# Kernel tuning notes

Measured on AMD Instinct MI355X. Metric: run time of the kernel, lower is better.

## Reference

```python
import jax, jax.numpy as jnp
import numpy as np
from jax import lax

NPOINT = 1024
NSAMPLE = 32
RADIUS = 0.6
BN_EPS = 1e-5


def square_distance(src, dst):
    # src (B,S,3), dst (B,N,3) -> (B,S,N) squared distances
    d = -2.0 * jnp.einsum('bsc,bnc->bsn', src, dst)
    d = d + jnp.sum(src ** 2, -1)[:, :, None]
    d = d + jnp.sum(dst ** 2, -1)[:, None, :]
    return d


def farthest_point_sample(xyz, npoint):
    B, N, _ = xyz.shape
    bidx = jnp.arange(B)

    def step(carry, _):
        distance, farthest = carry
        centroid = xyz[bidx, farthest]                      # (B,3)
        dist = jnp.sum((xyz - centroid[:, None, :]) ** 2, -1)  # (B,N)
        distance = jnp.minimum(distance, dist)
        new_far = jnp.argmax(distance, -1)
        return (distance, new_far), farthest

    init = (jnp.full((B, N), 1e10, xyz.dtype), jnp.zeros((B,), jnp.int32))
    _, idxs = lax.scan(step, init, None, length=npoint)
    return idxs.T                                            # (B,npoint)


def ball_query(xyz, new_xyz, radius, nsample):
    B, N, _ = xyz.shape
    sqr = square_distance(new_xyz, xyz)                      # (B,S,N)
    idx = jnp.where(sqr <= radius ** 2, jnp.arange(N)[None, None, :], N)
    idx = jnp.sort(idx, axis=-1)[:, :, :nsample]             # (B,S,K)
    first = idx[:, :, :1]
    return jnp.where(idx == N, first, idx)


def gather2(points, idx):
    # points (B,N,C), idx (B,S) -> (B,S,C)
    return jax.vmap(lambda p, i: p[i])(points, idx)


def gather3(points, idx):
    # points (B,N,C), idx (B,S,K) -> (B,S,K,C)
    return jax.vmap(lambda p, i: p[i])(points, idx)


def sa_forward(xyz, features, params):
    fps_idx = lax.stop_gradient(farthest_point_sample(xyz, NPOINT))
    new_xyz = gather2(xyz, fps_idx)                          # (B,S,3)
    idx = lax.stop_gradient(ball_query(xyz, new_xyz, RADIUS, NSAMPLE))
    grouped_xyz = gather3(xyz, idx) - new_xyz[:, :, None, :] # (B,S,K,3)
    grouped_feat = gather3(features.transpose(0, 2, 1), idx) # (B,S,K,C)
    g = jnp.concatenate([grouped_xyz, grouped_feat], -1)     # (B,S,K,C+3)
    g = g.transpose(0, 3, 2, 1)                              # (B,Cin,K,S)
    for w, b, ga, be in params:
        g = jnp.einsum('oc,bcks->boks', w, g) + b[None, :, None, None]
        mu = jnp.mean(g, axis=(0, 2, 3), keepdims=True)
        var = jnp.var(g, axis=(0, 2, 3), keepdims=True)
        g = ga[None, :, None, None] * (g - mu) * lax.rsqrt(var + BN_EPS) \
            + be[None, :, None, None]
        g = jax.nn.relu(g)
    new_features = jnp.max(g, axis=2)                        # (B,Cout,S)
    return new_xyz, new_features


def setup_inputs() -> dict:
    key = jax.random.key(0)
    ks = jax.random.split(key, 8)
    B, N, C = 16, 4096, 128
    cin = C + 3
    mlp = [128, 128, 256]
    inp = {
        'xyz': jax.random.normal(ks[0], (B, N, 3), jnp.float32),
        'features': jax.random.normal(ks[1], (B, C, N), jnp.float32),
    }
    prev = cin
    for i, out in enumerate(mlp):
        inp[f'w{i}'] = jax.random.normal(ks[2 + i], (out, prev), jnp.float32) * 0.05
        inp[f'b{i}'] = jnp.zeros((out,), jnp.float32)
        inp[f'gamma{i}'] = jnp.ones((out,), jnp.float32)
        inp[f'beta{i}'] = jnp.zeros((out,), jnp.float32)
        prev = out
    return inp


def reference(xyz, features, w0, b0, gamma0, beta0, w1, b1, gamma1, beta1,
              w2, b2, gamma2, beta2):
    params = [(w0, b0, gamma0, beta0), (w1, b1, gamma1, beta1),
              (w2, b2, gamma2, beta2)]
    return sa_forward(xyz, features, params)
```

## Files before the change

kernel.cpp:

```cpp
#include <hip/hip_runtime.h>

#define B_ 16
#define N_ 4096
#define S_ 1024
#define K_ 32
#define PITCH2 136
#define PITCH1 168

typedef unsigned long long u64;
typedef short bf16x8 __attribute__((ext_vector_type(8)));
typedef unsigned short u16x8 __attribute__((ext_vector_type(8)));
typedef float f32x4 __attribute__((ext_vector_type(4)));
typedef float f32x2 __attribute__((ext_vector_type(2)));

__device__ __forceinline__ unsigned short f2bf(float f) {
  unsigned u = __float_as_uint(f);
  unsigned r = (u + 0x7FFFu + ((u >> 16) & 1u)) >> 16;
  return (unsigned short)r;
}
__device__ __forceinline__ float bf2f(unsigned short h) {
  return __uint_as_float(((unsigned)h) << 16);
}

#define DPP_MAX(v, ctrl)                                                        \
  {                                                                             \
    int _t = __builtin_amdgcn_update_dpp(__float_as_int(v), __float_as_int(v),  \
                                         ctrl, 0xf, 0xf, false);                \
    v = fmaxf(v, __int_as_float(_t));                                           \
  }

__global__ __launch_bounds__(512) void k_front(
    const float* __restrict__ xyz, float* __restrict__ new_xyz,
    const float* __restrict__ feat, unsigned short* __restrict__ featT,
    const float* __restrict__ w0, const float* __restrict__ w1,
    const float* __restrict__ w2, unsigned short* __restrict__ wbf0,
    unsigned short* __restrict__ wbf1, unsigned short* __restrict__ wbf2,
    float* __restrict__ stats) {
  __shared__ __align__(16) float smem[N_ * 4 + S_ + 64];
  int blk = blockIdx.x, t = threadIdx.x;

  if (blk < 16) {
#pragma clang fp contract(off)
#if __has_builtin(__builtin_amdgcn_s_setprio)
    __builtin_amdgcn_s_setprio(3);
#endif
    float4* pts = (float4*)smem;
    int* idxs = (int*)(smem + N_ * 4);
    u64* km = (u64*)(smem + N_ * 4 + S_);
    int b = blk;
    const float* base = xyz + (size_t)b * N_ * 3;
    for (int i = t; i < N_; i += 512)
      pts[i] = make_float4(base[i * 3], base[i * 3 + 1], base[i * 3 + 2], 0.0f);
    if (t == 0) { idxs[0] = 0; km[0] = 0; km[1] = 0; km[2] = 0; }
    __syncthreads();
    f32x2 px[4], py[4], pz[4], pd[4];
    int i0 = t * 8;
    #pragma unroll
    for (int j = 0; j < 4; ++j) {
      float4 p0 = pts[i0 + 2 * j], p1 = pts[i0 + 2 * j + 1];
      px[j] = (f32x2){p0.x, p1.x};
      py[j] = (f32x2){p0.y, p1.y};
      pz[j] = (f32x2){p0.z, p1.z};
      pd[j] = (f32x2){1e10f, 1e10f};
    }
    int cur = 0;
    int sl = 0;
    for (int it = 0; it < S_; ++it) {
      float4 c = pts[cur];
      f32x2 c2x = (f32x2){c.x, c.x}, c2y = (f32x2){c.y, c.y}, c2z = (f32x2){c.z, c.z};
      float bestv = -1.0f; int besti = 0;
      #pragma unroll
      for (int j = 0; j < 4; ++j) {
        f32x2 dx = px[j] - c2x;
        f32x2 dy = py[j] - c2y;
        f32x2 dz = pz[j] - c2z;
        f32x2 d = (dx * dx + dy * dy) + dz * dz;
        f32x2 dm = __builtin_elementwise_min(pd[j], d);
        pd[j] = dm;
        if (dm.x > bestv) { bestv = dm.x; besti = 2 * j; }
        if (dm.y > bestv) { bestv = dm.y; besti = 2 * j + 1; }
      }
      float v = bestv;
      DPP_MAX(v, 0x111);
      DPP_MAX(v, 0x112);
      DPP_MAX(v, 0x114);
      DPP_MAX(v, 0x118);
      DPP_MAX(v, 0x142);
      DPP_MAX(v, 0x143);
      float wmax = __int_as_float(__builtin_amdgcn_readlane(__float_as_int(v), 63));
      u64 mask = __ballot(bestv == wmax);
      int owner = __ffsll((long long)mask) - 1;
      int widx = __builtin_amdgcn_readlane(i0 + besti, owner);
      if ((t & 63) == 0)
        atomicMax((unsigned long long*)&km[sl],
                  ((u64)__float_as_uint(wmax) << 32) | (unsigned)(4095 - widx));
      __syncthreads();
      u64 k0 = km[sl];
      cur = 4095 - (int)(unsigned)(k0 & 0xFFFFFFFFull);
      if (t == 0) {
        if (it + 1 < S_) idxs[it + 1] = cur;
        km[sl == 0 ? 2 : sl - 1] = 0;
      }
      sl = (sl == 2) ? 0 : sl + 1;
    }
    __syncthreads();
    for (int i = t; i < S_; i += 512) {
      float4 v = pts[idxs[i]];
      size_t o = ((size_t)b * S_ + i) * 3;
      new_xyz[o] = v.x; new_xyz[o + 1] = v.y; new_xyz[o + 2] = v.z;
    }
  } else if (blk < 32) {
    int id = (blk - 16) * 512 + t;
    const int st = 16 * 512;
    for (int i = id; i < 32768; i += st) stats[i] = 0.0f;
    for (int i = id; i < 128 * 160; i += st) {
      int n = i / 160, k = i - n * 160;
      float v = (k < 128) ? w0[n * 131 + 3 + k] : (k < 131) ? w0[n * 131 + k - 128] : 0.0f;
      wbf0[i] = f2bf(v);
    }
    for (int i = id; i < 128 * 128; i += st) wbf1[i] = f2bf(w1[i]);
    for (int i = id; i < 256 * 128; i += st) wbf2[i] = f2bf(w2[i]);
  } else {
    float (*tile)[33] = (float(*)[33])smem;
    int blk2 = blk - 32;
    int n0 = (blk2 & 127) * 32;
    int c0 = ((blk2 >> 7) & 3) * 32;
    int b = blk2 >> 9;
    int tx = t & 31, ty = t >> 5;
    #pragma unroll
    for (int j = 0; j < 32; j += 16)
      tile[ty + j][tx] = feat[((size_t)b * 128 + c0 + ty + j) * N_ + n0 + tx];
    __syncthreads();
    #pragma unroll
    for (int j = 0; j < 32; j += 16)
      featT[((size_t)b * N_ + n0 + ty + j) * 128 + c0 + tx] = f2bf(tile[tx][ty + j]);
  }
}

__global__ __launch_bounds__(256) void k_ballq(const float* __restrict__ xyz,
                                               const float* __restrict__ new_xyz,
                                               int* __restrict__ ball_idx) {
  int b = blockIdx.y;
  int s = blockIdx.x * 4 + (threadIdx.x >> 6);
  int lane = threadIdx.x & 63;
  const float* pb = xyz + (size_t)b * N_ * 3;
  size_t q = (size_t)b * S_ + s;
  float qx = new_xyz[q * 3], qy = new_xyz[q * 3 + 1], qz = new_xyz[q * 3 + 2];
  float sq = __fadd_rn(__fadd_rn(__fmul_rn(qx, qx), __fmul_rn(qy, qy)), __fmul_rn(qz, qz));
  int* out = ball_idx + q * K_;
  int total = 0;
  int first_idx = -1;
  for (int basei = 0; basei < N_; basei += 64) {
    int i = basei + lane;
    float fx = pb[i * 3], fy = pb[i * 3 + 1], fz = pb[i * 3 + 2];
    float dot = __fmul_rn(qx, fx);
    dot = __fadd_rn(dot, __fmul_rn(qy, fy));
    dot = __fadd_rn(dot, __fmul_rn(qz, fz));
    float sd = __fadd_rn(__fadd_rn(__fmul_rn(fx, fx), __fmul_rn(fy, fy)), __fmul_rn(fz, fz));
    float dist = __fadd_rn(__fadd_rn(__fmul_rn(-2.0f, dot), sq), sd);
    bool within = (dist <= 0.36f);
    u64 m = __ballot(within);
    if (first_idx < 0 && m) first_idx = basei + __ffsll((long long)m) - 1;
    if (within) {
      int pos = total + __popcll(m & ((1ull << lane) - 1ull));
      if (pos < K_) out[pos] = i;
    }
    total += (int)__popcll(m);
    if (total >= K_) break;
  }
  if (total < K_) {
    int k2 = total + lane;
    if (k2 < K_) out[k2] = first_idx;
  }
}

#define MFMA(a, b, c) __builtin_amdgcn_mfma_f32_16x16x32_bf16(a, b, c, 0, 0, 0)
#define NTILES 4096

__global__ __launch_bounds__(256) void k_layer1(
    const float* __restrict__ xyz, const float* __restrict__ new_xyz,
    const unsigned short* __restrict__ featT, const int* __restrict__ ball_idx,
    const unsigned short* __restrict__ wbf0, const float* __restrict__ b0,
    unsigned short* __restrict__ y, float* __restrict__ stats) {
  __shared__ __align__(16) unsigned short Wl[128 * PITCH1];
  __shared__ float sbias[128];
  int t = threadIdx.x;
  int w = t >> 6, L = t & 63, lm = L & 15, lg = L >> 4;
  {
    int n = t >> 1, h = t & 1;
    const uint4* wr = (const uint4*)(wbf0 + n * 160 + h * 80);
    uint4* wl = (uint4*)(Wl + n * PITCH1 + h * 80);
    #pragma unroll
    for (int i = 0; i < 10; ++i) wl[i] = wr[i];
    if (t < 128) sbias[t] = b0[t];
  }
  __syncthreads();

  for (int tile = blockIdx.x; tile < NTILES; tile += gridDim.x) {
    int bb = tile >> 8;
    int s0 = (tile & 255) * 4;
    size_t qg = (size_t)bb * S_ + s0 + w;

    int p0 = ball_idx[qg * K_ + lm];
    int p1 = ball_idx[qg * K_ + 16 + lm];
    const unsigned short* f0 = featT + ((size_t)bb * N_ + p0) * 128;
    const unsigned short* f1 = featT + ((size_t)bb * N_ + p1) * 128;
    bf16x8 a0[5], a1[5];
    #pragma unroll
    for (int kt = 0; kt < 4; ++kt) {
      a0[kt] = *(const bf16x8*)(f0 + kt * 32 + lg * 8);
      a1[kt] = *(const bf16x8*)(f1 + kt * 32 + lg * 8);
    }
    a0[4] = (bf16x8){0, 0, 0, 0, 0, 0, 0, 0};
    a1[4] = (bf16x8){0, 0, 0, 0, 0, 0, 0, 0};
    if (lg == 0) {
      float nx = new_xyz[qg * 3], ny = new_xyz[qg * 3 + 1], nz = new_xyz[qg * 3 + 2];
      const float* pp0 = xyz + ((size_t)bb * N_ + p0) * 3;
      const float* pp1 = xyz + ((size_t)bb * N_ + p1) * 3;
      a0[4][0] = (short)f2bf(pp0[0] - nx);
      a0[4][1] = (short)f2bf(pp0[1] - ny);
      a0[4][2] = (short)f2bf(pp0[2] - nz);
      a1[4][0] = (short)f2bf(pp1[0] - nx);
      a1[4][1] = (short)f2bf(pp1[1] - ny);
      a1[4][2] = (short)f2bf(pp1[2] - nz);
    }
    f32x4 acc[2][8];
    #pragma unroll
    for (int mi = 0; mi < 2; ++mi)
      #pragma unroll
      for (int nt = 0; nt < 8; ++nt) acc[mi][nt] = (f32x4){0.f, 0.f, 0.f, 0.f};
    #pragma unroll
    for (int kt = 0; kt < 5; ++kt) {
      int ko = kt * 32 + lg * 8;
      bf16x8 bv[8];
      #pragma unroll
      for (int nt = 0; nt < 8; ++nt)
        bv[nt] = *(const bf16x8*)&Wl[(nt * 16 + lm) * PITCH1 + ko];
      #pragma unroll
      for (int nt = 0; nt < 8; ++nt) {
        acc[0][nt] = MFMA(a0[kt], bv[nt], acc[0][nt]);
        acc[1][nt] = MFMA(a1[kt], bv[nt], acc[1][nt]);
      }
    }
    int slot = tile & 31;
    #pragma unroll
    for (int nt = 0; nt < 8; ++nt) {
      int col = nt * 16 + lm;
      float bo = sbias[col];
      float s1 = 0.f, s2 = 0.f;
      #pragma unroll
      for (int mi = 0; mi < 2; ++mi)
        #pragma unroll
        for (int r = 0; r < 4; ++r) {
          float yv = acc[mi][nt][r] + bo;
          s1 += yv; s2 += yv * yv;
          int ks = mi * 16 + lg * 4 + r;
          y[(qg * K_ + ks) * 128 + col] = f2bf(yv);
        }
      s1 += __shfl_xor(s1, 16); s2 += __shfl_xor(s2, 16);
      s1 += __shfl_xor(s1, 32); s2 += __shfl_xor(s2, 32);
      if (lg == 0) {
        atomicAdd(stats + ((size_t)slot * 128 + col) * 2, s1);
        atomicAdd(stats + ((size_t)slot * 128 + col) * 2 + 1, s2);
      }
    }
  }
}

__global__ __launch_bounds__(256) void k_layer2(
    unsigned short* y, const float* __restrict__ stats,
    const float* __restrict__ gamma, const float* __restrict__ beta,
    const unsigned short* __restrict__ wbf1, const float* __restrict__ b1,
    float* __restrict__ stats2) {
  __shared__ __align__(16) unsigned short Wl[128 * PITCH2];
  __shared__ __align__(16) float sa[128], sd[128];
  __shared__ float sbias[128];
  int t = threadIdx.x;
  int w = t >> 6, L = t & 63, lm = L & 15, lg = L >> 4;
  if (t < 128) {
    float s1 = 0.0f, s2 = 0.0f;
    for (int sl = 0; sl < 32; ++sl) {
      s1 += stats[((size_t)sl * 128 + t) * 2];
      s2 += stats[((size_t)sl * 128 + t) * 2 + 1];
    }
    const float inv = 1.0f / 524288.0f;
    float mu = s1 * inv;
    float var = s2 * inv - mu * mu;
    float a = gamma[t] * rsqrtf(var + 1e-5f);
    sa[t] = a;
    sd[t] = beta[t] - a * mu;
    sbias[t] = b1[t];
  }
  {
    int n = t >> 1, h = t & 1;
    const uint4* wr = (const uint4*)(wbf1 + n * 128 + h * 64);
    uint4* wl = (uint4*)(Wl + n * PITCH2 + h * 64);
    #pragma unroll
    for (int i = 0; i < 8; ++i) wl[i] = wr[i];
  }
  __syncthreads();

  for (int tile = blockIdx.x; tile < NTILES; tile += gridDim.x) {
    int bb = tile >> 8;
    int s0 = (tile & 255) * 4;
    size_t qg = (size_t)bb * S_ + s0 + w;

    const u16x8* yr0 = (const u16x8*)(y + (qg * K_ + lm) * 128);
    const u16x8* yr1 = (const u16x8*)(y + (qg * K_ + 16 + lm) * 128);
    u16x8 raw0[4], raw1[4];
    #pragma unroll
    for (int kt = 0; kt < 4; ++kt) { raw0[kt] = yr0[kt * 4 + lg]; raw1[kt] = yr1[kt * 4 + lg]; }
    bf16x8 a0[4], a1[4];
    #pragma unroll
    for (int kt = 0; kt < 4; ++kt) {
      int c = kt * 32 + lg * 8;
      f32x4 A0 = *(const f32x4*)&sa[c], A1 = *(const f32x4*)&sa[c + 4];
      f32x4 D0 = *(const f32x4*)&sd[c], D1 = *(const f32x4*)&sd[c + 4];
      #pragma unroll
      for (int j = 0; j < 4; ++j) {
        a0[kt][j]     = (short)f2bf(fmaxf(A0[j] * bf2f(raw0[kt][j])     + D0[j], 0.f));
        a0[kt][j + 4] = (short)f2bf(fmaxf(A1[j] * bf2f(raw0[kt][j + 4]) + D1[j], 0.f));
        a1[kt][j]     = (short)f2bf(fmaxf(A0[j] * bf2f(raw1[kt][j])     + D0[j], 0.f));
        a1[kt][j + 4] = (short)f2bf(fmaxf(A1[j] * bf2f(raw1[kt][j + 4]) + D1[j], 0.f));
      }
    }
    f32x4 acc[2][8];
    #pragma unroll
    for (int mi = 0; mi < 2; ++mi)
      #pragma unroll
      for (int nt = 0; nt < 8; ++nt) acc[mi][nt] = (f32x4){0.f, 0.f, 0.f, 0.f};
    #pragma unroll
    for (int kt = 0; kt < 4; ++kt) {
      int ko = kt * 32 + lg * 8;
      bf16x8 bv[8];
      #pragma unroll
      for (int nt = 0; nt < 8; ++nt)
        bv[nt] = *(const bf16x8*)&Wl[(nt * 16 + lm) * PITCH2 + ko];
      #pragma unroll
      for (int nt = 0; nt < 8; ++nt) {
        acc[0][nt] = MFMA(a0[kt], bv[nt], acc[0][nt]);
        acc[1][nt] = MFMA(a1[kt], bv[nt], acc[1][nt]);
      }
    }
    int slot = tile & 31;
    #pragma unroll
    for (int nt = 0; nt < 8; ++nt) {
      int col = nt * 16 + lm;
      float bo = sbias[col];
      float s1 = 0.f, s2 = 0.f;
      #pragma unroll
      for (int mi = 0; mi < 2; ++mi)
        #pragma unroll
        for (int r = 0; r < 4; ++r) {
          float yv = acc[mi][nt][r] + bo;
          s1 += yv; s2 += yv * yv;
          int ks = mi * 16 + lg * 4 + r;
          y[(qg * K_ + ks) * 128 + col] = f2bf(yv);
        }
      s1 += __shfl_xor(s1, 16); s2 += __shfl_xor(s2, 16);
      s1 += __shfl_xor(s1, 32); s2 += __shfl_xor(s2, 32);
      if (lg == 0) {
        atomicAdd(stats2 + ((size_t)slot * 128 + col) * 2, s1);
        atomicAdd(stats2 + ((size_t)slot * 128 + col) * 2 + 1, s2);
      }
    }
  }
}

__global__ __launch_bounds__(256) void k_layer3(
    const unsigned short* __restrict__ y, const float* __restrict__ stats2,
    const float* __restrict__ gamma, const float* __restrict__ beta,
    const unsigned short* __restrict__ wbf2, const float* __restrict__ b2,
    unsigned short* __restrict__ ymax, unsigned short* __restrict__ ymin,
    float* __restrict__ stats3) {
  __shared__ __align__(16) unsigned short Wl[128 * PITCH2];
  __shared__ __align__(16) float sa[128], sd[128];
  __shared__ float sbias[128];
  int nh = blockIdx.y, t = threadIdx.x;
  int w = t >> 6, L = t & 63, lm = L & 15, lg = L >> 4;
  if (t < 128) {
    float s1 = 0.0f, s2 = 0.0f;
    for (int sl = 0; sl < 32; ++sl) {
      s1 += stats2[((size_t)sl * 128 + t) * 2];
      s2 += stats2[((size_t)sl * 128 + t) * 2 + 1];
    }
    const float inv = 1.0f / 524288.0f;
    float mu = s1 * inv;
    float var = s2 * inv - mu * mu;
    float a = gamma[t] * rsqrtf(var + 1e-5f);
    sa[t] = a;
    sd[t] = beta[t] - a * mu;
    sbias[t] = b2[nh * 128 + t];
  }
  {
    int n = t >> 1, h = t & 1;
    const uint4* wr = (const uint4*)(wbf2 + (size_t)(nh * 128 + n) * 128 + h * 64);
    uint4* wl = (uint4*)(Wl + n * PITCH2 + h * 64);
    #pragma unroll
    for (int i = 0; i < 8; ++i) wl[i] = wr[i];
  }
  __syncthreads();

  for (int tile = blockIdx.x; tile < NTILES; tile += gridDim.x) {
    int bb = tile >> 8;
    int s0 = (tile & 255) * 4;
    size_t qg = (size_t)bb * S_ + s0 + w;

    const u16x8* yr0 = (const u16x8*)(y + (qg * K_ + lm) * 128);
    const u16x8* yr1 = (const u16x8*)(y + (qg * K_ + 16 + lm) * 128);
    u16x8 raw0[4], raw1[4];
    #pragma unroll
    for (int kt = 0; kt < 4; ++kt) { raw0[kt] = yr0[kt * 4 + lg]; raw1[kt] = yr1[kt * 4 + lg]; }
    bf16x8 a0[4], a1[4];
    #pragma unroll
    for (int kt = 0; kt < 4; ++kt) {
      int c = kt * 32 + lg * 8;
      f32x4 A0 = *(const f32x4*)&sa[c], A1 = *(const f32x4*)&sa[c + 4];
      f32x4 D0 = *(const f32x4*)&sd[c], D1 = *(const f32x4*)&sd[c + 4];
      #pragma unroll
      for (int j = 0; j < 4; ++j) {
        a0[kt][j]     = (short)f2bf(fmaxf(A0[j] * bf2f(raw0[kt][j])     + D0[j], 0.f));
        a0[kt][j + 4] = (short)f2bf(fmaxf(A1[j] * bf2f(raw0[kt][j + 4]) + D1[j], 0.f));
        a1[kt][j]     = (short)f2bf(fmaxf(A0[j] * bf2f(raw1[kt][j])     + D0[j], 0.f));
        a1[kt][j + 4] = (short)f2bf(fmaxf(A1[j] * bf2f(raw1[kt][j + 4]) + D1[j], 0.f));
      }
    }
    f32x4 acc[2][8];
    #pragma unroll
    for (int mi = 0; mi < 2; ++mi)
      #pragma unroll
      for (int nt = 0; nt < 8; ++nt) acc[mi][nt] = (f32x4){0.f, 0.f, 0.f, 0.f};
    #pragma unroll
    for (int kt = 0; kt < 4; ++kt) {
      int ko = kt * 32 + lg * 8;
      bf16x8 bv[8];
      #pragma unroll
      for (int nt = 0; nt < 8; ++nt)
        bv[nt] = *(const bf16x8*)&Wl[(nt * 16 + lm) * PITCH2 + ko];
      #pragma unroll
      for (int nt = 0; nt < 8; ++nt) {
        acc[0][nt] = MFMA(a0[kt], bv[nt], acc[0][nt]);
        acc[1][nt] = MFMA(a1[kt], bv[nt], acc[1][nt]);
      }
    }
    int slot = tile & 31;
    #pragma unroll
    for (int nt = 0; nt < 8; ++nt) {
      int col = nt * 16 + lm;
      int o = nh * 128 + col;
      float bo = sbias[col];
      float s1 = 0.f, s2 = 0.f, mx = -3.4e38f, mn = 3.4e38f;
      #pragma unroll
      for (int mi = 0; mi < 2; ++mi)
        #pragma unroll
        for (int r = 0; r < 4; ++r) {
          float yv = acc[mi][nt][r] + bo;
          s1 += yv; s2 += yv * yv;
          mx = fmaxf(mx, yv); mn = fminf(mn, yv);
        }
      s1 += __shfl_xor(s1, 16); s2 += __shfl_xor(s2, 16);
      s1 += __shfl_xor(s1, 32); s2 += __shfl_xor(s2, 32);
      mx = fmaxf(mx, __shfl_xor(mx, 16)); mx = fmaxf(mx, __shfl_xor(mx, 32));
      mn = fminf(mn, __shfl_xor(mn, 16)); mn = fminf(mn, __shfl_xor(mn, 32));
      if (lg == 0) {
        ymax[qg * 256 + o] = f2bf(mx);
        ymin[qg * 256 + o] = f2bf(mn);
        atomicAdd(stats3 + ((size_t)slot * 256 + o) * 2, s1);
        atomicAdd(stats3 + ((size_t)slot * 256 + o) * 2 + 1, s2);
      }
    }
  }
}

__global__ __launch_bounds__(256) void k_final(const unsigned short* __restrict__ ymax,
                                               const unsigned short* __restrict__ ymin,
                                               const float* __restrict__ stats3,
                                               const float* __restrict__ gamma,
                                               const float* __restrict__ beta,
                                               float* __restrict__ out2) {
  __shared__ float tile[32][33];
  __shared__ float smA[32], smD[32];
  int b = blockIdx.z, o0 = blockIdx.y * 32, s0 = blockIdx.x * 32;
  int tx = threadIdx.x, ty = threadIdx.y;
  if (ty == 0) {
    int c = o0 + tx;
    float s1 = 0.0f, s2 = 0.0f;
    for (int sl = 0; sl < 32; ++sl) {
      s1 += stats3[((size_t)sl * 256 + c) * 2];
      s2 += stats3[((size_t)sl * 256 + c) * 2 + 1];
    }
    const float inv = 1.0f / 524288.0f;
    float mu = s1 * inv;
    float var = s2 * inv - mu * mu;
    float a = gamma[c] * rsqrtf(var + 1e-5f);
    smA[tx] = a;
    smD[tx] = beta[c] - a * mu;
  }
  __syncthreads();
  float a_rd = smA[tx];
  #pragma unroll
  for (int j = 0; j < 32; j += 8) {
    size_t src = ((size_t)b * S_ + s0 + ty + j) * 256 + o0 + tx;
    tile[ty + j][tx] = (a_rd >= 0.0f) ? bf2f(ymax[src]) : bf2f(ymin[src]);
  }
  __syncthreads();
  #pragma unroll
  for (int j = 0; j < 32; j += 8) {
    float a = smA[ty + j], dd = smD[ty + j];
    out2[((size_t)b * 256 + o0 + ty + j) * S_ + s0 + tx] = fmaxf(a * tile[tx][ty + j] + dd, 0.0f);
  }
}

extern "C" void kernel_launch(void* const* d_in, const int* in_sizes, int n_in,
                              void* d_out, int out_size, void* d_ws, size_t ws_size,
                              hipStream_t stream) {
  (void)in_sizes; (void)n_in; (void)out_size; (void)ws_size;
  const float* xyz  = (const float*)d_in[0];
  const float* feat = (const float*)d_in[1];
  const float* w0   = (const float*)d_in[2];
  const float* b0   = (const float*)d_in[3];
  const float* ga0  = (const float*)d_in[4];
  const float* be0  = (const float*)d_in[5];
  const float* w1   = (const float*)d_in[6];
  const float* b1   = (const float*)d_in[7];
  const float* ga1  = (const float*)d_in[8];
  const float* be1  = (const float*)d_in[9];
  const float* w2   = (const float*)d_in[10];
  const float* b2   = (const float*)d_in[11];
  const float* ga2  = (const float*)d_in[12];
  const float* be2  = (const float*)d_in[13];

  float* out_xyz  = (float*)d_out;
  float* out_feat = out_xyz + (size_t)B_ * S_ * 3;

  char* ws = (char*)d_ws;
  size_t off = 0;
  auto alloc = [&](size_t bytes) -> void* {
    void* p = ws + off;
    off += (bytes + 255) & ~(size_t)255;
    return p;
  };
  unsigned short* featT = (unsigned short*)alloc((size_t)B_ * N_ * 128 * 2);
  int*   ball  = (int*)alloc((size_t)B_ * S_ * K_ * 4);
  float* stats = (float*)alloc(32768 * 4);
  unsigned short* wbf0 = (unsigned short*)alloc(128 * 160 * 2);
  unsigned short* wbf1 = (unsigned short*)alloc(128 * 128 * 2);
  unsigned short* wbf2 = (unsigned short*)alloc(256 * 128 * 2);
  unsigned short* ymaxb = (unsigned short*)alloc((size_t)B_ * S_ * 256 * 2);
  unsigned short* yminb = (unsigned short*)alloc((size_t)B_ * S_ * 256 * 2);
  unsigned short* y = (unsigned short*)alloc((size_t)B_ * S_ * K_ * 128 * 2);

  k_front<<<16 + 16 + 8192, 512, 0, stream>>>(xyz, out_xyz, feat, featT,
                                              w0, w1, w2, wbf0, wbf1, wbf2, stats);
  k_ballq<<<dim3(256, 16), 256, 0, stream>>>(xyz, out_xyz, ball);
  k_layer1<<<768, 256, 0, stream>>>(xyz, out_xyz, featT, ball, wbf0, b0, y, stats);
  k_layer2<<<1024, 256, 0, stream>>>(y, stats, ga0, be0, wbf1, b1, stats + 8192);
  k_layer3<<<dim3(512, 2), 256, 0, stream>>>(y, stats + 8192, ga1, be1, wbf2, b2,
                                             ymaxb, yminb, stats + 16384);
  k_final<<<dim3(32, 8, 16), dim3(32, 8), 0, stream>>>(ymaxb, yminb, stats + 16384,
                                                       ga2, be2, out_feat);
}
```

Baseline: 1.022 ms.

## Process both output halves per block in layer3 and shorten FPS wave reduction

Layer3 now computes all 256 output channels in one block: it loads the full weight matrix into shared memory and loops over two halves. Each activation tile is therefore read from global memory and normalised once, where before the two grid halves each did it. In FPS, the last two DPP reduction steps are replaced by four readlanes and a scalar unsigned max, which shortens the latency of the serial per-iteration argmax. The costs are doubled LDS use per block in layer3, which may lower occupancy, and half as many blocks in that grid.

New measurement: 978.9 us. 1.04x faster.

```diff
diff --git a/kernel.cpp b/kernel.cpp
--- a/kernel.cpp
+++ b/kernel.cpp
@@ -85,15 +85,20 @@
       DPP_MAX(v, 0x112);
       DPP_MAX(v, 0x114);
       DPP_MAX(v, 0x118);
-      DPP_MAX(v, 0x142);
-      DPP_MAX(v, 0x143);
-      float wmax = __int_as_float(__builtin_amdgcn_readlane(__float_as_int(v), 63));
+      unsigned r0 = (unsigned)__builtin_amdgcn_readlane(__float_as_int(v), 15);
+      unsigned r1 = (unsigned)__builtin_amdgcn_readlane(__float_as_int(v), 31);
+      unsigned r2 = (unsigned)__builtin_amdgcn_readlane(__float_as_int(v), 47);
+      unsigned r3 = (unsigned)__builtin_amdgcn_readlane(__float_as_int(v), 63);
+      unsigned ra = r0 > r1 ? r0 : r1;
+      unsigned rb = r2 > r3 ? r2 : r3;
+      unsigned wmaxb = ra > rb ? ra : rb;
+      float wmax = __uint_as_float(wmaxb);
       u64 mask = __ballot(bestv == wmax);
       int owner = __ffsll((long long)mask) - 1;
       int widx = __builtin_amdgcn_readlane(i0 + besti, owner);
       if ((t & 63) == 0)
         atomicMax((unsigned long long*)&km[sl],
-                  ((u64)__float_as_uint(wmax) << 32) | (unsigned)(4095 - widx));
+                  ((u64)wmaxb << 32) | (unsigned)(4095 - widx));
       __syncthreads();
       u64 k0 = km[sl];
       cur = 4095 - (int)(unsigned)(k0 & 0xFFFFFFFFull);
@@ -373,10 +378,10 @@
     const unsigned short* __restrict__ wbf2, const float* __restrict__ b2,
     unsigned short* __restrict__ ymax, unsigned short* __restrict__ ymin,
     float* __restrict__ stats3) {
-  __shared__ __align__(16) unsigned short Wl[128 * PITCH2];
+  __shared__ __align__(16) unsigned short Wl[256 * PITCH2];
   __shared__ __align__(16) float sa[128], sd[128];
-  __shared__ float sbias[128];
-  int nh = blockIdx.y, t = threadIdx.x;
+  __shared__ float sbias[256];
+  int t = threadIdx.x;
   int w = t >> 6, L = t & 63, lm = L & 15, lg = L >> 4;
   if (t < 128) {
     float s1 = 0.0f, s2 = 0.0f;
@@ -390,14 +395,13 @@
     float a = gamma[t] * rsqrtf(var + 1e-5f);
     sa[t] = a;
     sd[t] = beta[t] - a * mu;
-    sbias[t] = b2[nh * 128 + t];
-  }
+  }
+  sbias[t] = b2[t];
   {
-    int n = t >> 1, h = t & 1;
-    const uint4* wr = (const uint4*)(wbf2 + (size_t)(nh * 128 + n) * 128 + h * 64);
-    uint4* wl = (uint4*)(Wl + n * PITCH2 + h * 64);
-    #pragma unroll
-    for (int i = 0; i < 8; ++i) wl[i] = wr[i];
+    const uint4* wr = (const uint4*)(wbf2 + (size_t)t * 128);
+    uint4* wl = (uint4*)(Wl + t * PITCH2);
+    #pragma unroll
+    for (int i = 0; i < 16; ++i) wl[i] = wr[i];
   }
   __syncthreads();
 
@@ -425,48 +429,51 @@
         a1[kt][j + 4] = (short)f2bf(fmaxf(A1[j] * bf2f(raw1[kt][j + 4]) + D1[j], 0.f));
       }
     }
-    f32x4 acc[2][8];
-    #pragma unroll
-    for (int mi = 0; mi < 2; ++mi)
-      #pragma unroll
-      for (int nt = 0; nt < 8; ++nt) acc[mi][nt] = (f32x4){0.f, 0.f, 0.f, 0.f};
-    #pragma unroll
-    for (int kt = 0; kt < 4; ++kt) {
-      int ko = kt * 32 + lg * 8;
-      bf16x8 bv[8];
-      #pragma unroll
-      for (int nt = 0; nt < 8; ++nt)
-        bv[nt] = *(const bf16x8*)&Wl[(nt * 16 + lm) * PITCH2 + ko];
-      #pragma unroll
-      for (int nt = 0; nt < 8; ++nt) {
-        acc[0][nt] = MFMA(a0[kt], bv[nt], acc[0][nt]);
-        acc[1][nt] = MFMA(a1[kt], bv[nt], acc[1][nt]);
-      }
-    }
     int slot = tile & 31;
     #pragma unroll
-    for (int nt = 0; nt < 8; ++nt) {
-      int col = nt * 16 + lm;
-      int o = nh * 128 + col;
-      float bo = sbias[col];
-      float s1 = 0.f, s2 = 0.f, mx = -3.4e38f, mn = 3.4e38f;
+    for (int h = 0; h < 2; ++h) {
+      f32x4 acc[2][8];
       #pragma unroll
       for (int mi = 0; mi < 2; ++mi)
         #pragma unroll
-        for (int r = 0; r < 4; ++r) {
-          float yv = acc[mi][nt][r] + bo;
-          s1 += yv; s2 += yv * yv;
-          mx = fmaxf(mx, yv); mn = fminf(mn, yv);
+        for (int nt = 0; nt < 8; ++nt) acc[mi][nt] = (f32x4){0.f, 0.f, 0.f, 0.f};
+      #pragma unroll
+      for (int kt = 0; kt < 4; ++kt) {
+        int ko = kt * 32 + lg * 8;
+        bf16x8 bv[8];
+        #pragma unroll
+        for (int nt = 0; nt < 8; ++nt)
+          bv[nt] = *(const bf16x8*)&Wl[(h * 128 + nt * 16 + lm) * PITCH2 + ko];
+        #pragma unroll
+        for (int nt = 0; nt < 8; ++nt) {
+          acc[0][nt] = MFMA(a0[kt], bv[nt], acc[0][nt]);
+          acc[1][nt] = MFMA(a1[kt], bv[nt], acc[1][nt]);
         }
-      s1 += __shfl_xor(s1, 16); s2 += __shfl_xor(s2, 16);
-      s1 += __shfl_xor(s1, 32); s2 += __shfl_xor(s2, 32);
-      mx = fmaxf(mx, __shfl_xor(mx, 16)); mx = fmaxf(mx, __shfl_xor(mx, 32));
-      mn = fminf(mn, __shfl_xor(mn, 16)); mn = fminf(mn, __shfl_xor(mn, 32));
-      if (lg == 0) {
-        ymax[qg * 256 + o] = f2bf(mx);
-        ymin[qg * 256 + o] = f2bf(mn);
-        atomicAdd(stats3 + ((size_t)slot * 256 + o) * 2, s1);
-        atomicAdd(stats3 + ((size_t)slot * 256 + o) * 2 + 1, s2);
+      }
+      #pragma unroll
+      for (int nt = 0; nt < 8; ++nt) {
+        int col = nt * 16 + lm;
+        int o = h * 128 + col;
+        float bo = sbias[o];
+        float s1 = 0.f, s2 = 0.f, mx = -3.4e38f, mn = 3.4e38f;
+        #pragma unroll
+        for (int mi = 0; mi < 2; ++mi)
+          #pragma unroll
+          for (int r = 0; r < 4; ++r) {
+            float yv = acc[mi][nt][r] + bo;
+            s1 += yv; s2 += yv * yv;
+            mx = fmaxf(mx, yv); mn = fminf(mn, yv);
+          }
+        s1 += __shfl_xor(s1, 16); s2 += __shfl_xor(s2, 16);
+        s1 += __shfl_xor(s1, 32); s2 += __shfl_xor(s2, 32);
+        mx = fmaxf(mx, __shfl_xor(mx, 16)); mx = fmaxf(mx, __shfl_xor(mx, 32));
+        mn = fminf(mn, __shfl_xor(mn, 16)); mn = fminf(mn, __shfl_xor(mn, 32));
+        if (lg == 0) {
+          ymax[qg * 256 + o] = f2bf(mx);
+          ymin[qg * 256 + o] = f2bf(mn);
+          atomicAdd(stats3 + ((size_t)slot * 256 + o) * 2, s1);
+          atomicAdd(stats3 + ((size_t)slot * 256 + o) * 2 + 1, s2);
+        }
       }
     }
   }
@@ -555,8 +562,8 @@
   k_ballq<<<dim3(256, 16), 256, 0, stream>>>(xyz, out_xyz, ball);
   k_layer1<<<768, 256, 0, stream>>>(xyz, out_xyz, featT, ball, wbf0, b0, y, stats);
   k_layer2<<<1024, 256, 0, stream>>>(y, stats, ga0, be0, wbf1, b1, stats + 8192);
-  k_layer3<<<dim3(512, 2), 256, 0, stream>>>(y, stats + 8192, ga1, be1, wbf2, b2,
-                                             ymaxb, yminb, stats + 16384);
+  k_layer3<<<512, 256, 0, stream>>>(y, stats + 8192, ga1, be1, wbf2, b2,
+                                    ymaxb, yminb, stats + 16384);
   k_final<<<dim3(32, 8, 16), dim3(32, 8), 0, stream>>>(ymaxb, yminb, stats + 16384,
                                                        ga2, be2, out_feat);
 }
```
